# Optimization experiments

Measured on AMD Instinct MI355X. Metric: run time of the kernel, lower is better.

## Reference

```python
import jax, jax.numpy as jnp
import numpy as np

B, N1, N2, D, L, H = 2, 384, 384, 128, 3, 128
DM_MIN = 0.5


def _gat_layer(x, adj, W, Wb, A, gW, gb):
    # GAT_gate from jaechanglim/DTI_PDBbind: attention softmax over dim 1, gated residual
    h = x @ W + Wb                                   # [B,N,D]
    e = jnp.einsum('bjl,bkl->bjk', h @ A, h)
    e = e + jnp.swapaxes(e, 1, 2)
    att = jnp.where(adj > 0, e, -9e15)
    att = jax.nn.softmax(att, axis=1) * adj
    h_prime = jax.nn.relu(jnp.einsum('bij,bjk->bik', att, h))
    coeff = jax.nn.sigmoid(jnp.concatenate([x, h_prime], -1) @ gW + gb)  # [B,N,1]
    return coeff * x + (1.0 - coeff) * h_prime


def _pair_mlp(h1g, h2g, W1, b1, W2, b2):
    # MLP(concat(h1_i, h2_j)) without materializing the [B,N1,N2,2D] concat:
    # split W1 into ligand / protein halves and broadcast-add the projections.
    p1 = jnp.einsum('bnd,dk->bnk', h1g, W1[:D])      # [B,N1,H]
    p2 = jnp.einsum('bmd,dk->bmk', h2g, W1[D:])      # [B,N2,H]
    hid = jax.nn.relu(p1[:, :, None, :] + p2[:, None, :, :] + b1)  # [B,N1,N2,H]
    return (hid @ W2 + b2)[..., 0]                   # [B,N1,N2]


def reference(h1, adj1, h2, dmv, charge1, charge2, vdw_epsilon, vdw_sigma,
              delta_uff, valid1, valid2, no_metal1, no_metal2,
              node_W, gat_W, gat_Wb, gat_A, gat_gW, gat_gb,
              pair_W1, pair_b1, pair_W2, pair_b2,
              vdw_coeff, duff_coeff, int_W1, int_b1, int_W2, int_b2):
    h1g = h1 @ node_W
    h2g = h2 @ node_W
    for i in range(L):  # only ligand graph is convolved (as in the source)
        h1g = _gat_layer(h1g, adj1, gat_W[i], gat_Wb[i], gat_A[i], gat_gW[i], gat_gb[i])

    dm = jnp.sqrt(jnp.sum(dmv * dmv, -1) + 1e-10)    # [B,N1,N2]
    dm = jnp.where(dm < DM_MIN, 1e10, dm)

    # coulomb term (pair MLPs 0,1)
    cA = jax.nn.sigmoid(_pair_mlp(h1g, h2g, pair_W1[0], pair_b1[0], pair_W2[0], pair_b2[0]))
    cN = jax.nn.sigmoid(_pair_mlp(h1g, h2g, pair_W1[1], pair_b1[1], pair_W2[1], pair_b2[1])) * 2.0 + 1.0
    charge12 = charge1[:, :, None] * charge2[:, None, :]
    e_c = cA * charge12 * jnp.power(1.0 / dm, cN)
    e_c = e_c * valid1[:, :, None] * valid2[:, None, :]
    e_c = jnp.clip(e_c, -100.0, 100.0)
    e_c = jnp.sum(e_c, axis=(1, 2))[:, None]

    # vdw term (pair MLPs 2=A sigmoid, 3=B tanh, 4=N sigmoid)
    vA = (jax.nn.sigmoid(_pair_mlp(h1g, h2g, pair_W1[2], pair_b1[2], pair_W2[2], pair_b2[2])) * 0.6 + 0.7)
    vA = vA * (vdw_coeff[0] * vdw_coeff[0]) * vdw_epsilon
    vB = jnp.tanh(_pair_mlp(h1g, h2g, pair_W1[3], pair_b1[3], pair_W2[3], pair_b2[3])) * 0.6 + 0.7
    vN = jax.nn.sigmoid(_pair_mlp(h1g, h2g, pair_W1[4], pair_b1[4], pair_W2[4], pair_b2[4])) * 2.0 + 5.0
    dm0 = vdw_sigma * vB
    dm0 = jnp.where(dm0 < 1e-4, 1.0, dm0)
    r = jnp.power(dm0 / dm, vN)
    e_v = vA * (r * r - 2.0 * r)                     # (dm0/dm)^(2N) - 2(dm0/dm)^N
    e_v = e_v * no_metal1[:, :, None] * no_metal2[:, None, :]
    e_v = jnp.minimum(e_v, 100.0)
    e_v = jnp.sum(e_v, axis=(1, 2))[:, None]

    # conformational energy difference term
    e_u = (duff_coeff[0] * duff_coeff[0] * delta_uff)[:, None]

    # learned intercept from pooled ligand features
    hs = jnp.sum(h1g * valid1[..., None], axis=1)
    inter = jax.nn.relu(hs @ int_W1 + int_b1) @ int_W2 + int_b2

    return jnp.concatenate([e_c, e_v, e_u, inter], -1)  # [B,4]


def setup_inputs() -> dict:
    key = jax.random.key(0)
    ks = jax.random.split(key, 24)
    inp = {}
    inp['h1'] = jax.random.normal(ks[0], (B, N1, 54), jnp.float32)
    inp['h2'] = jax.random.normal(ks[1], (B, N2, 54), jnp.float32)
    a = jax.random.uniform(ks[2], (B, N1, N1))
    adj = (a > 0.9).astype(jnp.float32)
    adj = jnp.maximum(adj, jnp.swapaxes(adj, 1, 2))
    inp['adj1'] = jnp.maximum(adj, jnp.eye(N1, dtype=jnp.float32)[None])
    inp['dmv'] = jax.random.normal(ks[3], (B, N1, N2, 3), jnp.float32) * 3.0
    inp['charge1'] = jax.random.normal(ks[4], (B, N1), jnp.float32) * 0.3
    inp['charge2'] = jax.random.normal(ks[5], (B, N2), jnp.float32) * 0.3
    inp['vdw_epsilon'] = jax.random.uniform(ks[6], (B, N1, N2), jnp.float32) * 0.3
    inp['vdw_sigma'] = 3.0 + jax.random.uniform(ks[7], (B, N1, N2), jnp.float32)
    inp['delta_uff'] = jax.random.uniform(ks[8], (B,), jnp.float32) * 5.0
    inp['valid1'] = jnp.ones((B, N1), jnp.float32)
    inp['valid2'] = jnp.ones((B, N2), jnp.float32)
    inp['no_metal1'] = jnp.ones((B, N1), jnp.float32)
    inp['no_metal2'] = jnp.ones((B, N2), jnp.float32)
    # parameters
    inp['node_W'] = jax.random.normal(ks[9], (54, D), jnp.float32) * 0.1
    inp['gat_W'] = jax.random.normal(ks[10], (L, D, D), jnp.float32) * (1.0 / np.sqrt(D))
    inp['gat_Wb'] = jnp.zeros((L, D), jnp.float32)
    inp['gat_A'] = jax.random.normal(ks[11], (L, D, D), jnp.float32) * 0.05
    inp['gat_gW'] = jax.random.normal(ks[12], (L, 2 * D, 1), jnp.float32) * 0.05
    inp['gat_gb'] = jnp.zeros((L, 1), jnp.float32)
    inp['pair_W1'] = jax.random.normal(ks[13], (5, 2 * D, H), jnp.float32) * 0.05
    inp['pair_b1'] = jnp.zeros((5, H), jnp.float32)
    inp['pair_W2'] = jax.random.normal(ks[14], (5, H, 1), jnp.float32) * 0.1
    inp['pair_b2'] = jnp.zeros((5, 1), jnp.float32)
    inp['vdw_coeff'] = jnp.array([0.02], jnp.float32)
    inp['duff_coeff'] = jnp.array([0.1], jnp.float32)
    inp['int_W1'] = jax.random.normal(ks[15], (D, H), jnp.float32) * 0.05
    inp['int_b1'] = jnp.zeros((H,), jnp.float32)
    inp['int_W2'] = jax.random.normal(ks[16], (H, 1), jnp.float32) * 0.1
    inp['int_b2'] = jnp.zeros((1,), jnp.float32)
    return inp
```

## Files before the change

kernel.cpp:

```cpp
#include <hip/hip_runtime.h>
#include <math.h>

#define BB 2
#define NN 384
#define DD 128
#define HH 128
#define RT_ALL (BB * NN)
#define PCOLS (BB * NN)

__device__ __forceinline__ float sigmoidf_(float x) { return 1.f / (1.f + __expf(-x)); }
__device__ __forceinline__ float tanhf_(float x)    { return 1.f - 2.f / (__expf(2.f * x) + 1.f); }

__global__ __launch_bounds__(256) void k_embed(
    const float* __restrict__ h1, const float* __restrict__ h2,
    const float* __restrict__ nW, float* __restrict__ h1g, float* __restrict__ h2g) {
  int r0 = blockIdx.x * 2;
  int tid = threadIdx.x;
  const float* src; float* dst; int rb;
  if (r0 < RT_ALL) { src = h1; dst = h1g; rb = r0; }
  else             { src = h2; dst = h2g; rb = r0 - RT_ALL; }
  __shared__ float xs[2][54];
  if (tid < 108) xs[tid / 54][tid % 54] = src[rb * 54 + tid];
  __syncthreads();
  int rr = tid >> 7, c = tid & 127;
  float acc = 0.f;
#pragma unroll 6
  for (int k = 0; k < 54; ++k) acc += xs[rr][k] * nW[k * DD + c];
  dst[(rb + rr) * DD + c] = acc;
}

__global__ __launch_bounds__(256) void k_gat_hhA(
    const float* __restrict__ x, const float* __restrict__ W,
    const float* __restrict__ Wb, const float* __restrict__ A,
    float* __restrict__ h, float* __restrict__ hA,
    float* __restrict__ hT, float* __restrict__ hAT) {
  int r = blockIdx.x;
  int tid = threadIdx.x, c = tid & 127, kh = tid >> 7;
  __shared__ float xs[DD], hs[DD];
  __shared__ float ph[2][DD];
  if (tid < DD) xs[tid] = x[r * DD + tid];
  __syncthreads();
  float acc = 0.f;
  const float* Wp = W + (kh * 64) * DD + c;
#pragma unroll 4
  for (int k = 0; k < 64; ++k) acc += xs[kh * 64 + k] * Wp[k * DD];
  ph[kh][c] = acc;
  __syncthreads();
  if (tid < DD) {
    float hv = ph[0][tid] + ph[1][tid] + Wb[tid];
    h[r * DD + tid] = hv; hT[tid * PCOLS + r] = hv; hs[tid] = hv;
  }
  __syncthreads();
  acc = 0.f;
  const float* Ap = A + (kh * 64) * DD + c;
#pragma unroll 4
  for (int k = 0; k < 64; ++k) acc += hs[kh * 64 + k] * Ap[k * DD];
  ph[kh][c] = acc;
  __syncthreads();
  if (tid < DD) {
    float av = ph[0][tid] + ph[1][tid];
    hA[r * DD + tid] = av; hAT[tid * PCOLS + r] = av;
  }
}

__global__ __launch_bounds__(384) void k_gat_att(
    const float* __restrict__ h, const float* __restrict__ hA,
    const float* __restrict__ hT, const float* __restrict__ hAT,
    const float* __restrict__ adj, float* __restrict__ attT) {
  int col = blockIdx.x;
  int b = col / NN;
  int tid = threadIdx.x;
  const float* hrow  = h  + col * DD;
  const float* hArow = hA + col * DD;
  const float* hTb  = hT  + b * NN + tid;
  const float* hATb = hAT + b * NN + tid;
  float e = 0.f;
#pragma unroll 8
  for (int c = 0; c < DD; ++c)
    e += hATb[c * PCOLS] * hrow[c] + hTb[c * PCOLS] * hArow[c];
  float a = adj[col * NN + tid];
  __shared__ float rmx[6], rsm[6];
  float lmax = (a > 0.f) ? e : -3e38f;
#pragma unroll
  for (int off = 32; off > 0; off >>= 1) lmax = fmaxf(lmax, __shfl_down(lmax, off));
  if ((tid & 63) == 0) rmx[tid >> 6] = lmax;
  __syncthreads();
  float m = fmaxf(fmaxf(fmaxf(rmx[0], rmx[1]), fmaxf(rmx[2], rmx[3])), fmaxf(rmx[4], rmx[5]));
  float v = (a > 0.f) ? __expf(e - m) : 0.f;
  float s = v;
#pragma unroll
  for (int off = 32; off > 0; off >>= 1) s += __shfl_down(s, off);
  if ((tid & 63) == 0) rsm[tid >> 6] = s;
  __syncthreads();
  float inv = 1.f / (rsm[0] + rsm[1] + rsm[2] + rsm[3] + rsm[4] + rsm[5]);
  attT[col * NN + tid] = v * a * inv;
}

__global__ __launch_bounds__(256) void k_gat_out(
    const float* __restrict__ x, const float* __restrict__ h,
    const float* __restrict__ attT, const float* __restrict__ gW,
    const float* __restrict__ gb, float* __restrict__ out) {
  int r = blockIdx.x;
  int b = r / NN, i = r - b * NN;
  int tid = threadIdx.x, c = tid & 127, jh = tid >> 7;
  __shared__ float arow[NN];
  __shared__ float ph[2][DD];
  __shared__ float redw[2];
  for (int idx = tid; idx < NN; idx += 256) arow[idx] = attT[(b * NN + idx) * NN + i];
  __syncthreads();
  float acc = 0.f;
  const float* hp = h + (b * NN + jh * 192) * DD + c;
#pragma unroll 4
  for (int jj = 0; jj < 192; ++jj) acc += arow[jh * 192 + jj] * hp[jj * DD];
  ph[jh][c] = acc;
  __syncthreads();
  if (tid < DD) {
    float hpr = fmaxf(ph[0][tid] + ph[1][tid], 0.f);
    float xr = x[r * DD + tid];
    float v = xr * gW[tid] + hpr * gW[DD + tid];
#pragma unroll
    for (int off = 32; off > 0; off >>= 1) v += __shfl_down(v, off);
    if ((tid & 63) == 0) redw[tid >> 6] = v;
  }
  __syncthreads();
  if (tid < DD) {
    float hpr = fmaxf(ph[0][tid] + ph[1][tid], 0.f);
    float xr = x[r * DD + tid];
    float coeff = sigmoidf_(redw[0] + redw[1] + gb[0]);
    out[r * DD + tid] = coeff * xr + (1.f - coeff) * hpr;
  }
}

__global__ __launch_bounds__(256) void k_pair_proj(
    const float* __restrict__ h1g, const float* __restrict__ h2g,
    const float* __restrict__ W1, const float* __restrict__ b1,
    const float* __restrict__ delta_uff, const float* __restrict__ duff_coeff,
    float* __restrict__ p1, float* __restrict__ p2T, float* __restrict__ out) {
  const int RT = 16;
  int m = blockIdx.x % 5;
  int r0 = (blockIdx.x / 5) * RT;
  int tid = threadIdx.x, c = tid & 127, kh = tid >> 7;
  if (blockIdx.x == 0 && tid < BB * 4) {
    int bb = tid >> 2, cc = tid & 3;
    out[tid] = (cc == 2) ? duff_coeff[0] * duff_coeff[0] * delta_uff[bb] : 0.f;
  }
  bool lig = (r0 < RT_ALL);
  const float* src = lig ? h1g : h2g;
  int rb = lig ? r0 : r0 - RT_ALL;
  const float* W = W1 + (m * 256 + (lig ? 0 : 128)) * HH;
  __shared__ float xs[RT][DD];
  __shared__ float ps[RT][DD];
  for (int idx = tid; idx < RT * DD; idx += 256) xs[idx >> 7][idx & 127] = src[rb * DD + idx];
  __syncthreads();
  float acc[RT];
#pragma unroll
  for (int r = 0; r < RT; ++r) acc[r] = 0.f;
  const float* Wp = W + (kh * 64) * HH + c;
#pragma unroll 2
  for (int k = 0; k < 64; ++k) {
    float w = Wp[k * HH];
#pragma unroll
    for (int r = 0; r < RT; ++r) acc[r] += xs[r][kh * 64 + k] * w;
  }
  if (kh == 1) {
#pragma unroll
    for (int r = 0; r < RT; ++r) ps[r][c] = acc[r];
  }
  __syncthreads();
  if (kh == 0) {
    if (lig) {
      float bias = b1[m * HH + c];
#pragma unroll
      for (int r = 0; r < RT; ++r)
        p1[((rb + r) * 5 + m) * HH + c] = acc[r] + ps[r][c] + bias;
    } else {
      float* dst = p2T + (m * HH + c) * PCOLS + rb;
#pragma unroll
      for (int q = 0; q < RT / 4; ++q) {
        float4 v = make_float4(acc[4 * q + 0] + ps[4 * q + 0][c],
                               acc[4 * q + 1] + ps[4 * q + 1][c],
                               acc[4 * q + 2] + ps[4 * q + 2][c],
                               acc[4 * q + 3] + ps[4 * q + 3][c]);
        *(float4*)(dst + 4 * q) = v;
      }
    }
  }
}

__global__ __launch_bounds__(192) void k_pair_energy(
    const float* __restrict__ p1, const float* __restrict__ p2T,
    const float* __restrict__ W2, const float* __restrict__ b2,
    const float* __restrict__ dmv, const float* __restrict__ charge1,
    const float* __restrict__ charge2, const float* __restrict__ veps,
    const float* __restrict__ vsig, const float* __restrict__ valid1,
    const float* __restrict__ valid2, const float* __restrict__ nm1,
    const float* __restrict__ nm2, const float* __restrict__ vdw_coeff,
    const float* __restrict__ h1g, float* __restrict__ ws_int,
    float* __restrict__ out) {
  int tid = threadIdx.x;
  if (blockIdx.x >= 768) {
    int eb = blockIdx.x - 768;
    int b = eb >> 2, ch = eb & 3;
    if (tid < DD) {
      float acc = 0.f;
      int i0 = ch * 96;
#pragma unroll 4
      for (int i = 0; i < 96; ++i) {
        int gi = b * NN + i0 + i;
        acc += h1g[gi * DD + tid] * valid1[gi];
      }
      ws_int[eb * DD + tid] = acc;
    }
    return;
  }
  const int TI = 2;
  int tile = blockIdx.x >> 1, jh = blockIdx.x & 1;
  int r0 = tile * TI;
  int b = r0 / NN;
  int j = jh * 192 + tid;
  int col = b * NN + j;

  const float* q0 = p1 + (r0 + 0) * 5 * HH;
  const float* q1 = p1 + (r0 + 1) * 5 * HH;
  float acc0[5], acc1[5];
#pragma unroll
  for (int m = 0; m < 5; ++m) {
    const float* p2c = p2T + m * HH * PCOLS + col;
    const float* w2m = W2 + m * HH;
    const float* x0 = q0 + m * HH;
    const float* x1 = q1 + m * HH;
    float a0 = b2[m], a1 = b2[m];
#pragma unroll 8
    for (int h = 0; h < HH; ++h) {
      float pv = p2c[h * PCOLS];
      float w = w2m[h];
      a0 += fmaxf(x0[h] + pv, 0.f) * w;
      a1 += fmaxf(x1[h] + pv, 0.f) * w;
    }
    acc0[m] = a0; acc1[m] = a1;
  }

  float q2c = charge2[col], v2 = valid2[col], n2 = nm2[col];
  float vc2 = vdw_coeff[0] * vdw_coeff[0];
  float ec_sum = 0.f, ev_sum = 0.f;
#pragma unroll
  for (int ti = 0; ti < TI; ++ti) {
    const float* am = ti ? acc1 : acc0;
    int gi = r0 + ti;
    int pidx = gi * NN + j;
    float dx = dmv[pidx * 3 + 0], dy = dmv[pidx * 3 + 1], dz = dmv[pidx * 3 + 2];
    float dm = sqrtf(dx * dx + dy * dy + dz * dz + 1e-10f);
    if (dm < 0.5f) dm = 1e10f;
    float cA = sigmoidf_(am[0]);
    float cN = sigmoidf_(am[1]) * 2.f + 1.f;
    float e_c = cA * charge1[gi] * q2c * __powf(1.f / dm, cN);
    e_c *= valid1[gi] * v2;
    e_c = fminf(fmaxf(e_c, -100.f), 100.f);
    ec_sum += e_c;
    float vA = (sigmoidf_(am[2]) * 0.6f + 0.7f) * vc2 * veps[pidx];
    float vB = tanhf_(am[3]) * 0.6f + 0.7f;
    float vN = sigmoidf_(am[4]) * 2.f + 5.f;
    float dm0 = vsig[pidx] * vB;
    if (dm0 < 1e-4f) dm0 = 1.f;
    float rr = __powf(dm0 / dm, vN);
    float e_v = vA * (rr * rr - 2.f * rr);
    e_v *= nm1[gi] * n2;
    e_v = fminf(e_v, 100.f);
    ev_sum += e_v;
  }
#pragma unroll
  for (int off = 32; off > 0; off >>= 1) {
    ec_sum += __shfl_down(ec_sum, off);
    ev_sum += __shfl_down(ev_sum, off);
  }
  __shared__ float rec[3], rev[3];
  if ((tid & 63) == 0) { rec[tid >> 6] = ec_sum; rev[tid >> 6] = ev_sum; }
  __syncthreads();
  if (tid == 0) {
    atomicAdd(&out[b * 4 + 0], rec[0] + rec[1] + rec[2]);
    atomicAdd(&out[b * 4 + 1], rev[0] + rev[1] + rev[2]);
  }
}

__global__ __launch_bounds__(256) void k_intercept_fin(
    const float* __restrict__ ws_int, const float* __restrict__ W1,
    const float* __restrict__ b1, const float* __restrict__ W2,
    const float* __restrict__ b2, float* __restrict__ out) {
  int b = blockIdx.x;
  int tid = threadIdx.x, c = tid & 127, kh = tid >> 7;
  __shared__ float hsf[DD];
  __shared__ float ph[2][DD];
  __shared__ float redw[2];
  if (tid < DD)
    hsf[tid] = ws_int[(b * 4 + 0) * DD + tid] + ws_int[(b * 4 + 1) * DD + tid]
             + ws_int[(b * 4 + 2) * DD + tid] + ws_int[(b * 4 + 3) * DD + tid];
  __syncthreads();
  float acc = 0.f;
  const float* Wp = W1 + (kh * 64) * HH + c;
#pragma unroll 4
  for (int k = 0; k < 64; ++k) acc += hsf[kh * 64 + k] * Wp[k * HH];
  ph[kh][c] = acc;
  __syncthreads();
  if (tid < DD) {
    float hid = fmaxf(ph[0][tid] + ph[1][tid] + b1[tid], 0.f);
    float v = hid * W2[tid];
#pragma unroll
    for (int off = 32; off > 0; off >>= 1) v += __shfl_down(v, off);
    if ((tid & 63) == 0) redw[tid >> 6] = v;
  }
  __syncthreads();
  if (tid == 0) out[b * 4 + 3] = redw[0] + redw[1] + b2[0];
}

extern "C" void kernel_launch(void* const* d_in, const int* in_sizes, int n_in,
                              void* d_out, int out_size, void* d_ws, size_t ws_size,
                              hipStream_t stream) {
  (void)in_sizes; (void)n_in; (void)out_size; (void)ws_size;
  const float* h1         = (const float*)d_in[0];
  const float* h2         = (const float*)d_in[1];
  const float* adj1       = (const float*)d_in[2];
  const float* dmv        = (const float*)d_in[3];
  const float* charge1    = (const float*)d_in[4];
  const float* charge2    = (const float*)d_in[5];
  const float* veps       = (const float*)d_in[6];
  const float* vsig       = (const float*)d_in[7];
  const float* delta_uff  = (const float*)d_in[8];
  const float* valid1     = (const float*)d_in[9];
  const float* valid2     = (const float*)d_in[10];
  const float* nm1        = (const float*)d_in[11];
  const float* nm2        = (const float*)d_in[12];
  const float* node_W     = (const float*)d_in[13];
  const float* gat_W      = (const float*)d_in[14];
  const float* gat_Wb     = (const float*)d_in[15];
  const float* gat_A      = (const float*)d_in[16];
  const float* gat_gW     = (const float*)d_in[17];
  const float* gat_gb     = (const float*)d_in[18];
  const float* pW1        = (const float*)d_in[19];
  const float* pb1        = (const float*)d_in[20];
  const float* pW2        = (const float*)d_in[21];
  const float* pb2        = (const float*)d_in[22];
  const float* vdw_coeff  = (const float*)d_in[23];
  const float* duff_coeff = (const float*)d_in[24];
  const float* iW1        = (const float*)d_in[25];
  const float* ib1        = (const float*)d_in[26];
  const float* iW2        = (const float*)d_in[27];
  const float* ib2        = (const float*)d_in[28];
  float* out = (float*)d_out;

  float* ws = (float*)d_ws;
  const int RN = BB * NN * DD;
  float* h1gA   = ws;
  float* h1gB   = h1gA + RN;
  float* h2g    = h1gB + RN;
  float* hbuf   = h2g + RN;
  float* hAbuf  = hbuf + RN;
  float* hTbuf  = hAbuf + RN;
  float* hATbuf = hTbuf + RN;
  float* attT   = hATbuf + RN;
  float* p1     = attT + BB * NN * NN;
  float* p2T    = p1 + BB * NN * 5 * HH;
  float* ws_int = p2T + 5 * HH * PCOLS;

  k_embed<<<dim3(2 * BB * NN / 2), dim3(256), 0, stream>>>(h1, h2, node_W, h1gA, h2g);

  float* cur = h1gA;
  float* nxt = h1gB;
  for (int l = 0; l < 3; ++l) {
    k_gat_hhA<<<dim3(BB * NN), dim3(256), 0, stream>>>(
        cur, gat_W + l * DD * DD, gat_Wb + l * DD, gat_A + l * DD * DD,
        hbuf, hAbuf, hTbuf, hATbuf);
    k_gat_att<<<dim3(BB * NN), dim3(384), 0, stream>>>(
        hbuf, hAbuf, hTbuf, hATbuf, adj1, attT);
    k_gat_out<<<dim3(BB * NN), dim3(256), 0, stream>>>(
        cur, hbuf, attT, gat_gW + l * 2 * DD, gat_gb + l, nxt);
    float* t = cur; cur = nxt; nxt = t;
  }
  const float* h1gF = cur;

  k_pair_proj<<<dim3((2 * BB * NN / 16) * 5), dim3(256), 0, stream>>>(
      h1gF, h2g, pW1, pb1, delta_uff, duff_coeff, p1, p2T, out);
  k_pair_energy<<<dim3(768 + 8), dim3(192), 0, stream>>>(
      p1, p2T, pW2, pb2, dmv, charge1, charge2, veps, vsig,
      valid1, valid2, nm1, nm2, vdw_coeff, h1gF, ws_int, out);
  k_intercept_fin<<<dim3(BB), dim3(256), 0, stream>>>(ws_int, iW1, ib1, iW2, ib2, out);
}
```

Measured before the change: 325.7 us.

## Fuse all stages into one cooperative persistent kernel with grid syncs

Replaces the chain of about thirteen separate kernel launches with a single cooperative kernel of 256 blocks that moves from stage to stage using grid.sync(). Each stage is re-tiled so every block handles three or six rows, and the pair-energy stage reads the protein projection through a float4-interleaved layout. The aim is to remove launch gaps and per-launch overhead. In exchange the grid is small (256 blocks), each row's work is serialised across fewer threads, and every grid-wide barrier adds its own cost.

Result: slower. 761.1 us (+133.7%).

```diff
diff --git a/kernel.cpp b/kernel.cpp
--- a/kernel.cpp
+++ b/kernel.cpp
@@ -1,386 +1,385 @@
 #include <hip/hip_runtime.h>
+#include <hip/hip_cooperative_groups.h>
 #include <math.h>
 
-#define BB 2
+namespace cg = cooperative_groups;
+
 #define NN 384
 #define DD 128
 #define HH 128
-#define RT_ALL (BB * NN)
-#define PCOLS (BB * NN)
 
 __device__ __forceinline__ float sigmoidf_(float x) { return 1.f / (1.f + __expf(-x)); }
 __device__ __forceinline__ float tanhf_(float x)    { return 1.f - 2.f / (__expf(2.f * x) + 1.f); }
 
-__global__ __launch_bounds__(256) void k_embed(
-    const float* __restrict__ h1, const float* __restrict__ h2,
-    const float* __restrict__ nW, float* __restrict__ h1g, float* __restrict__ h2g) {
-  int r0 = blockIdx.x * 2;
-  int tid = threadIdx.x;
-  const float* src; float* dst; int rb;
-  if (r0 < RT_ALL) { src = h1; dst = h1g; rb = r0; }
-  else             { src = h2; dst = h2g; rb = r0 - RT_ALL; }
-  __shared__ float xs[2][54];
-  if (tid < 108) xs[tid / 54][tid % 54] = src[rb * 54 + tid];
-  __syncthreads();
-  int rr = tid >> 7, c = tid & 127;
-  float acc = 0.f;
+struct Params {
+  const float *h1, *h2, *adj1, *dmv, *charge1, *charge2, *veps, *vsig, *delta_uff;
+  const float *valid1, *valid2, *nm1, *nm2;
+  const float *node_W, *gat_W, *gat_Wb, *gat_A, *gat_gW, *gat_gb;
+  const float *pW1, *pb1, *pW2, *pb2, *vdw_coeff, *duff_coeff;
+  const float *iW1, *ib1, *iW2, *ib2;
+  float *out;
+  float *h1gA, *h1gB, *h2g, *hbuf, *hAbuf, *hTbuf, *hATbuf, *att, *p1, *p2q, *ws_int;
+};
+
+__global__ __launch_bounds__(384) void k_mega(Params P) {
+  cg::grid_group grid = cg::this_grid();
+  const int blk = blockIdx.x;
+  const int tid = threadIdx.x;
+  const int c = tid & 127;
+  const int g = tid >> 7;
+
+  if (blk == 0 && tid < 8) {
+    int bb = tid >> 2, cc = tid & 3;
+    P.out[tid] = (cc == 2) ? P.duff_coeff[0] * P.duff_coeff[0] * P.delta_uff[bb] : 0.f;
+  }
+  {
+    int rb = blk * 6;
+    for (int p = 0; p < 2; ++p) {
+      int r = rb + p * 3 + g;
+      const float* src; float* dst; int rr;
+      if (r < 768) { src = P.h1; dst = P.h1gA; rr = r; }
+      else         { src = P.h2; dst = P.h2g;  rr = r - 768; }
+      const float* xr = src + rr * 54;
+      float acc = 0.f;
 #pragma unroll 6
-  for (int k = 0; k < 54; ++k) acc += xs[rr][k] * nW[k * DD + c];
-  dst[(rb + rr) * DD + c] = acc;
-}
-
-__global__ __launch_bounds__(256) void k_gat_hhA(
-    const float* __restrict__ x, const float* __restrict__ W,
-    const float* __restrict__ Wb, const float* __restrict__ A,
-    float* __restrict__ h, float* __restrict__ hA,
-    float* __restrict__ hT, float* __restrict__ hAT) {
-  int r = blockIdx.x;
-  int tid = threadIdx.x, c = tid & 127, kh = tid >> 7;
-  __shared__ float xs[DD], hs[DD];
-  __shared__ float ph[2][DD];
-  if (tid < DD) xs[tid] = x[r * DD + tid];
-  __syncthreads();
-  float acc = 0.f;
-  const float* Wp = W + (kh * 64) * DD + c;
-#pragma unroll 4
-  for (int k = 0; k < 64; ++k) acc += xs[kh * 64 + k] * Wp[k * DD];
-  ph[kh][c] = acc;
-  __syncthreads();
-  if (tid < DD) {
-    float hv = ph[0][tid] + ph[1][tid] + Wb[tid];
-    h[r * DD + tid] = hv; hT[tid * PCOLS + r] = hv; hs[tid] = hv;
-  }
-  __syncthreads();
-  acc = 0.f;
-  const float* Ap = A + (kh * 64) * DD + c;
-#pragma unroll 4
-  for (int k = 0; k < 64; ++k) acc += hs[kh * 64 + k] * Ap[k * DD];
-  ph[kh][c] = acc;
-  __syncthreads();
-  if (tid < DD) {
-    float av = ph[0][tid] + ph[1][tid];
-    hA[r * DD + tid] = av; hAT[tid * PCOLS + r] = av;
-  }
-}
-
-__global__ __launch_bounds__(384) void k_gat_att(
-    const float* __restrict__ h, const float* __restrict__ hA,
-    const float* __restrict__ hT, const float* __restrict__ hAT,
-    const float* __restrict__ adj, float* __restrict__ attT) {
-  int col = blockIdx.x;
-  int b = col / NN;
-  int tid = threadIdx.x;
-  const float* hrow  = h  + col * DD;
-  const float* hArow = hA + col * DD;
-  const float* hTb  = hT  + b * NN + tid;
-  const float* hATb = hAT + b * NN + tid;
-  float e = 0.f;
-#pragma unroll 8
-  for (int c = 0; c < DD; ++c)
-    e += hATb[c * PCOLS] * hrow[c] + hTb[c * PCOLS] * hArow[c];
-  float a = adj[col * NN + tid];
-  __shared__ float rmx[6], rsm[6];
-  float lmax = (a > 0.f) ? e : -3e38f;
-#pragma unroll
-  for (int off = 32; off > 0; off >>= 1) lmax = fmaxf(lmax, __shfl_down(lmax, off));
-  if ((tid & 63) == 0) rmx[tid >> 6] = lmax;
-  __syncthreads();
-  float m = fmaxf(fmaxf(fmaxf(rmx[0], rmx[1]), fmaxf(rmx[2], rmx[3])), fmaxf(rmx[4], rmx[5]));
-  float v = (a > 0.f) ? __expf(e - m) : 0.f;
-  float s = v;
-#pragma unroll
-  for (int off = 32; off > 0; off >>= 1) s += __shfl_down(s, off);
-  if ((tid & 63) == 0) rsm[tid >> 6] = s;
-  __syncthreads();
-  float inv = 1.f / (rsm[0] + rsm[1] + rsm[2] + rsm[3] + rsm[4] + rsm[5]);
-  attT[col * NN + tid] = v * a * inv;
-}
-
-__global__ __launch_bounds__(256) void k_gat_out(
-    const float* __restrict__ x, const float* __restrict__ h,
-    const float* __restrict__ attT, const float* __restrict__ gW,
-    const float* __restrict__ gb, float* __restrict__ out) {
-  int r = blockIdx.x;
-  int b = r / NN, i = r - b * NN;
-  int tid = threadIdx.x, c = tid & 127, jh = tid >> 7;
-  __shared__ float arow[NN];
-  __shared__ float ph[2][DD];
-  __shared__ float redw[2];
-  for (int idx = tid; idx < NN; idx += 256) arow[idx] = attT[(b * NN + idx) * NN + i];
-  __syncthreads();
-  float acc = 0.f;
-  const float* hp = h + (b * NN + jh * 192) * DD + c;
-#pragma unroll 4
-  for (int jj = 0; jj < 192; ++jj) acc += arow[jh * 192 + jj] * hp[jj * DD];
-  ph[jh][c] = acc;
-  __syncthreads();
-  if (tid < DD) {
-    float hpr = fmaxf(ph[0][tid] + ph[1][tid], 0.f);
-    float xr = x[r * DD + tid];
-    float v = xr * gW[tid] + hpr * gW[DD + tid];
-#pragma unroll
-    for (int off = 32; off > 0; off >>= 1) v += __shfl_down(v, off);
-    if ((tid & 63) == 0) redw[tid >> 6] = v;
-  }
-  __syncthreads();
-  if (tid < DD) {
-    float hpr = fmaxf(ph[0][tid] + ph[1][tid], 0.f);
-    float xr = x[r * DD + tid];
-    float coeff = sigmoidf_(redw[0] + redw[1] + gb[0]);
-    out[r * DD + tid] = coeff * xr + (1.f - coeff) * hpr;
-  }
-}
-
-__global__ __launch_bounds__(256) void k_pair_proj(
-    const float* __restrict__ h1g, const float* __restrict__ h2g,
-    const float* __restrict__ W1, const float* __restrict__ b1,
-    const float* __restrict__ delta_uff, const float* __restrict__ duff_coeff,
-    float* __restrict__ p1, float* __restrict__ p2T, float* __restrict__ out) {
-  const int RT = 16;
-  int m = blockIdx.x % 5;
-  int r0 = (blockIdx.x / 5) * RT;
-  int tid = threadIdx.x, c = tid & 127, kh = tid >> 7;
-  if (blockIdx.x == 0 && tid < BB * 4) {
-    int bb = tid >> 2, cc = tid & 3;
-    out[tid] = (cc == 2) ? duff_coeff[0] * duff_coeff[0] * delta_uff[bb] : 0.f;
-  }
-  bool lig = (r0 < RT_ALL);
-  const float* src = lig ? h1g : h2g;
-  int rb = lig ? r0 : r0 - RT_ALL;
-  const float* W = W1 + (m * 256 + (lig ? 0 : 128)) * HH;
-  __shared__ float xs[RT][DD];
-  __shared__ float ps[RT][DD];
-  for (int idx = tid; idx < RT * DD; idx += 256) xs[idx >> 7][idx & 127] = src[rb * DD + idx];
-  __syncthreads();
-  float acc[RT];
-#pragma unroll
-  for (int r = 0; r < RT; ++r) acc[r] = 0.f;
-  const float* Wp = W + (kh * 64) * HH + c;
-#pragma unroll 2
-  for (int k = 0; k < 64; ++k) {
-    float w = Wp[k * HH];
-#pragma unroll
-    for (int r = 0; r < RT; ++r) acc[r] += xs[r][kh * 64 + k] * w;
-  }
-  if (kh == 1) {
-#pragma unroll
-    for (int r = 0; r < RT; ++r) ps[r][c] = acc[r];
-  }
-  __syncthreads();
-  if (kh == 0) {
-    if (lig) {
-      float bias = b1[m * HH + c];
-#pragma unroll
-      for (int r = 0; r < RT; ++r)
-        p1[((rb + r) * 5 + m) * HH + c] = acc[r] + ps[r][c] + bias;
-    } else {
-      float* dst = p2T + (m * HH + c) * PCOLS + rb;
-#pragma unroll
-      for (int q = 0; q < RT / 4; ++q) {
-        float4 v = make_float4(acc[4 * q + 0] + ps[4 * q + 0][c],
-                               acc[4 * q + 1] + ps[4 * q + 1][c],
-                               acc[4 * q + 2] + ps[4 * q + 2][c],
-                               acc[4 * q + 3] + ps[4 * q + 3][c]);
-        *(float4*)(dst + 4 * q) = v;
-      }
-    }
-  }
-}
-
-__global__ __launch_bounds__(192) void k_pair_energy(
-    const float* __restrict__ p1, const float* __restrict__ p2T,
-    const float* __restrict__ W2, const float* __restrict__ b2,
-    const float* __restrict__ dmv, const float* __restrict__ charge1,
-    const float* __restrict__ charge2, const float* __restrict__ veps,
-    const float* __restrict__ vsig, const float* __restrict__ valid1,
-    const float* __restrict__ valid2, const float* __restrict__ nm1,
-    const float* __restrict__ nm2, const float* __restrict__ vdw_coeff,
-    const float* __restrict__ h1g, float* __restrict__ ws_int,
-    float* __restrict__ out) {
-  int tid = threadIdx.x;
-  if (blockIdx.x >= 768) {
-    int eb = blockIdx.x - 768;
-    int b = eb >> 2, ch = eb & 3;
-    if (tid < DD) {
+      for (int k = 0; k < 54; ++k) acc += xr[k] * P.node_W[k * DD + c];
+      dst[rr * DD + c] = acc;
+    }
+  }
+  grid.sync();
+
+  float* cur = P.h1gA;
+  float* nxt = P.h1gB;
+  for (int l = 0; l < 3; ++l) {
+    const float* W  = P.gat_W  + l * DD * DD;
+    const float* Wb = P.gat_Wb + l * DD;
+    const float* A  = P.gat_A  + l * DD * DD;
+    const float* gW = P.gat_gW + l * 2 * DD;
+    const float* gb = P.gat_gb + l;
+
+    {
+      __shared__ float hs[3][DD];
+      int r = blk * 3 + g;
+      const float4* xr4 = (const float4*)(cur + r * DD);
+      float a0 = 0.f, a1 = 0.f;
+#pragma unroll 4
+      for (int k4 = 0; k4 < DD / 4; ++k4) {
+        float4 xv = xr4[k4];
+        int k = k4 * 4;
+        a0 += xv.x * W[k * DD + c] + xv.z * W[(k + 2) * DD + c];
+        a1 += xv.y * W[(k + 1) * DD + c] + xv.w * W[(k + 3) * DD + c];
+      }
+      float hv = a0 + a1 + Wb[c];
+      P.hbuf[r * DD + c] = hv;
+      P.hTbuf[c * 768 + r] = hv;
+      hs[g][c] = hv;
+      __syncthreads();
+      const float4* hs4 = (const float4*)hs[g];
+      a0 = 0.f; a1 = 0.f;
+#pragma unroll 4
+      for (int k4 = 0; k4 < DD / 4; ++k4) {
+        float4 xv = hs4[k4];
+        int k = k4 * 4;
+        a0 += xv.x * A[k * DD + c] + xv.z * A[(k + 2) * DD + c];
+        a1 += xv.y * A[(k + 1) * DD + c] + xv.w * A[(k + 3) * DD + c];
+      }
+      float av = a0 + a1;
+      P.hAbuf[r * DD + c] = av;
+      P.hATbuf[c * 768 + r] = av;
+    }
+    grid.sync();
+
+    {
+      __shared__ float red[3][6];
+      int b = blk >> 7;
+      int k0g = blk * 3;
+      int kk0 = k0g - b * NN;
+      int j = tid;
+      const float* hTb  = P.hTbuf  + b * NN + j;
+      const float* hATb = P.hATbuf + b * NN + j;
+      const float* h0r = P.hbuf  + (k0g + 0) * DD;
+      const float* h1r = P.hbuf  + (k0g + 1) * DD;
+      const float* h2r = P.hbuf  + (k0g + 2) * DD;
+      const float* a0r = P.hAbuf + (k0g + 0) * DD;
+      const float* a1r = P.hAbuf + (k0g + 1) * DD;
+      const float* a2r = P.hAbuf + (k0g + 2) * DD;
+      float e0 = 0.f, e1 = 0.f, e2 = 0.f;
+#pragma unroll 4
+      for (int cc = 0; cc < DD; ++cc) {
+        float tv = hTb[cc * 768], av = hATb[cc * 768];
+        e0 += av * h0r[cc] + tv * a0r[cc];
+        e1 += av * h1r[cc] + tv * a1r[cc];
+        e2 += av * h2r[cc] + tv * a2r[cc];
+      }
+      float aj0 = P.adj1[(k0g + 0) * NN + j];
+      float aj1 = P.adj1[(k0g + 1) * NN + j];
+      float aj2 = P.adj1[(k0g + 2) * NN + j];
+      float l0 = aj0 > 0.f ? e0 : -3e38f;
+      float l1 = aj1 > 0.f ? e1 : -3e38f;
+      float l2 = aj2 > 0.f ? e2 : -3e38f;
+#pragma unroll
+      for (int off = 32; off > 0; off >>= 1) {
+        l0 = fmaxf(l0, __shfl_down(l0, off));
+        l1 = fmaxf(l1, __shfl_down(l1, off));
+        l2 = fmaxf(l2, __shfl_down(l2, off));
+      }
+      int w = tid >> 6;
+      if ((tid & 63) == 0) { red[0][w] = l0; red[1][w] = l1; red[2][w] = l2; }
+      __syncthreads();
+      float m0 = red[0][0], m1 = red[1][0], m2 = red[2][0];
+#pragma unroll
+      for (int q = 1; q < 6; ++q) {
+        m0 = fmaxf(m0, red[0][q]); m1 = fmaxf(m1, red[1][q]); m2 = fmaxf(m2, red[2][q]);
+      }
+      float v0 = aj0 > 0.f ? __expf(e0 - m0) : 0.f;
+      float v1 = aj1 > 0.f ? __expf(e1 - m1) : 0.f;
+      float v2 = aj2 > 0.f ? __expf(e2 - m2) : 0.f;
+      float s0 = v0, s1 = v1, s2 = v2;
+#pragma unroll
+      for (int off = 32; off > 0; off >>= 1) {
+        s0 += __shfl_down(s0, off);
+        s1 += __shfl_down(s1, off);
+        s2 += __shfl_down(s2, off);
+      }
+      __syncthreads();
+      if ((tid & 63) == 0) { red[0][w] = s0; red[1][w] = s1; red[2][w] = s2; }
+      __syncthreads();
+      float d0 = 0.f, d1 = 0.f, d2 = 0.f;
+#pragma unroll
+      for (int q = 0; q < 6; ++q) { d0 += red[0][q]; d1 += red[1][q]; d2 += red[2][q]; }
+      float* arow = P.att + (b * NN + j) * NN + kk0;
+      arow[0] = v0 * aj0 / d0;
+      arow[1] = v1 * aj1 / d1;
+      arow[2] = v2 * aj2 / d2;
+    }
+    grid.sync();
+
+    {
+      __shared__ float redw[3][2];
+      int r = blk * 3 + g;
+      int b = blk >> 7;
+      const float4* ar4 = (const float4*)(P.att + r * NN);
+      const float* hp = P.hbuf + b * NN * DD + c;
+      float q0 = 0.f, q1 = 0.f, q2 = 0.f, q3 = 0.f;
+#pragma unroll 4
+      for (int j4 = 0; j4 < NN / 4; ++j4) {
+        float4 av = ar4[j4];
+        const float* hj = hp + j4 * 4 * DD;
+        q0 += av.x * hj[0];
+        q1 += av.y * hj[DD];
+        q2 += av.z * hj[2 * DD];
+        q3 += av.w * hj[3 * DD];
+      }
+      float hpr = fmaxf((q0 + q1) + (q2 + q3), 0.f);
+      float xr = cur[r * DD + c];
+      float v = xr * gW[c] + hpr * gW[DD + c];
+#pragma unroll
+      for (int off = 32; off > 0; off >>= 1) v += __shfl_down(v, off);
+      if ((tid & 63) == 0) redw[g][(tid >> 6) & 1] = v;
+      __syncthreads();
+      float coeff = sigmoidf_(redw[g][0] + redw[g][1] + gb[0]);
+      nxt[r * DD + c] = coeff * xr + (1.f - coeff) * hpr;
+    }
+    { float* t = cur; cur = nxt; nxt = t; }
+    grid.sync();
+  }
+
+  {
+    bool lig = blk < 128;
+    int rbase = lig ? blk * 6 : blk * 6 - 768;
+    const float* src = lig ? cur : P.h2g;
+    const float* xbase = src + rbase * DD;
+    for (int pass = 0; pass < 2; ++pass) {
+      int o = tid + pass * 384;
+      if (o < 640) {
+        int m = o >> 7, hc = o & 127;
+        const float* Wcol = P.pW1 + (m * 256 + (lig ? 0 : 128)) * HH + hc;
+        float acc[6] = {0.f, 0.f, 0.f, 0.f, 0.f, 0.f};
+#pragma unroll 4
+        for (int k = 0; k < DD; ++k) {
+          float w = Wcol[k * HH];
+#pragma unroll
+          for (int r = 0; r < 6; ++r) acc[r] += xbase[r * DD + k] * w;
+        }
+        if (lig) {
+          float bias = P.pb1[m * HH + hc];
+#pragma unroll
+          for (int r = 0; r < 6; ++r)
+            P.p1[((rbase + r) * 5 + m) * HH + hc] = acc[r] + bias;
+        } else {
+          float* dst = P.p2q + (size_t)((m * 32 + (hc >> 2)) * 768 + rbase) * 4 + (hc & 3);
+#pragma unroll
+          for (int r = 0; r < 6; ++r) dst[4 * r] = acc[r];
+        }
+      }
+    }
+  }
+  grid.sync();
+
+  {
+    int b = blk >> 7;
+    int r0 = blk * 3;
+    int j = tid;
+    int col = b * NN + j;
+    const float* q0 = P.p1 + (r0 + 0) * 640;
+    const float* q1 = P.p1 + (r0 + 1) * 640;
+    const float* q2 = P.p1 + (r0 + 2) * 640;
+    const float4* p2q4 = (const float4*)P.p2q;
+    float am[3][5];
+#pragma unroll
+    for (int m = 0; m < 5; ++m) {
+      const float4* pc = p2q4 + (size_t)(m * 32) * 768 + col;
+      const float* w2m = P.pW2 + m * HH;
+      const float* x0 = q0 + m * HH;
+      const float* x1 = q1 + m * HH;
+      const float* x2 = q2 + m * HH;
+      float a0 = 0.f, a1 = 0.f, a2 = 0.f;
+#pragma unroll 4
+      for (int hq = 0; hq < 32; ++hq) {
+        float4 pv = pc[(size_t)hq * 768];
+        float w0 = w2m[4 * hq], w1 = w2m[4 * hq + 1], w2v = w2m[4 * hq + 2], w3 = w2m[4 * hq + 3];
+        a0 += fmaxf(x0[4 * hq] + pv.x, 0.f) * w0 + fmaxf(x0[4 * hq + 1] + pv.y, 0.f) * w1
+            + fmaxf(x0[4 * hq + 2] + pv.z, 0.f) * w2v + fmaxf(x0[4 * hq + 3] + pv.w, 0.f) * w3;
+        a1 += fmaxf(x1[4 * hq] + pv.x, 0.f) * w0 + fmaxf(x1[4 * hq + 1] + pv.y, 0.f) * w1
+            + fmaxf(x1[4 * hq + 2] + pv.z, 0.f) * w2v + fmaxf(x1[4 * hq + 3] + pv.w, 0.f) * w3;
+        a2 += fmaxf(x2[4 * hq] + pv.x, 0.f) * w0 + fmaxf(x2[4 * hq + 1] + pv.y, 0.f) * w1
+            + fmaxf(x2[4 * hq + 2] + pv.z, 0.f) * w2v + fmaxf(x2[4 * hq + 3] + pv.w, 0.f) * w3;
+      }
+      float bb = P.pb2[m];
+      am[0][m] = a0 + bb; am[1][m] = a1 + bb; am[2][m] = a2 + bb;
+    }
+
+    float q2c = P.charge2[col], vv2 = P.valid2[col], n2 = P.nm2[col];
+    float vc2 = P.vdw_coeff[0] * P.vdw_coeff[0];
+    float ec_sum = 0.f, ev_sum = 0.f;
+#pragma unroll
+    for (int ti = 0; ti < 3; ++ti) {
+      int gi = r0 + ti;
+      int pidx = gi * NN + j;
+      float dx = P.dmv[pidx * 3], dy = P.dmv[pidx * 3 + 1], dz = P.dmv[pidx * 3 + 2];
+      float dm = sqrtf(dx * dx + dy * dy + dz * dz + 1e-10f);
+      if (dm < 0.5f) dm = 1e10f;
+      float cA = sigmoidf_(am[ti][0]);
+      float cN = sigmoidf_(am[ti][1]) * 2.f + 1.f;
+      float e_c = cA * P.charge1[gi] * q2c * __powf(1.f / dm, cN);
+      e_c *= P.valid1[gi] * vv2;
+      e_c = fminf(fmaxf(e_c, -100.f), 100.f);
+      ec_sum += e_c;
+      float vA = (sigmoidf_(am[ti][2]) * 0.6f + 0.7f) * vc2 * P.veps[pidx];
+      float vB = tanhf_(am[ti][3]) * 0.6f + 0.7f;
+      float vN = sigmoidf_(am[ti][4]) * 2.f + 5.f;
+      float dm0 = P.vsig[pidx] * vB;
+      if (dm0 < 1e-4f) dm0 = 1.f;
+      float rr = __powf(dm0 / dm, vN);
+      float e_v = vA * (rr * rr - 2.f * rr);
+      e_v *= P.nm1[gi] * n2;
+      e_v = fminf(e_v, 100.f);
+      ev_sum += e_v;
+    }
+#pragma unroll
+    for (int off = 32; off > 0; off >>= 1) {
+      ec_sum += __shfl_down(ec_sum, off);
+      ev_sum += __shfl_down(ev_sum, off);
+    }
+    __shared__ float rec[6], rev[6];
+    if ((tid & 63) == 0) { rec[tid >> 6] = ec_sum; rev[tid >> 6] = ev_sum; }
+    __syncthreads();
+    if (tid == 0) {
+      float a = 0.f, cc = 0.f;
+#pragma unroll
+      for (int w = 0; w < 6; ++w) { a += rec[w]; cc += rev[w]; }
+      atomicAdd(&P.out[b * 4 + 0], a);
+      atomicAdd(&P.out[b * 4 + 1], cc);
+    }
+    if (blk < 8 && tid < DD) {
+      int bb = blk >> 2, ch = blk & 3;
       float acc = 0.f;
       int i0 = ch * 96;
 #pragma unroll 4
       for (int i = 0; i < 96; ++i) {
-        int gi = b * NN + i0 + i;
-        acc += h1g[gi * DD + tid] * valid1[gi];
-      }
-      ws_int[eb * DD + tid] = acc;
-    }
-    return;
-  }
-  const int TI = 2;
-  int tile = blockIdx.x >> 1, jh = blockIdx.x & 1;
-  int r0 = tile * TI;
-  int b = r0 / NN;
-  int j = jh * 192 + tid;
-  int col = b * NN + j;
-
-  const float* q0 = p1 + (r0 + 0) * 5 * HH;
-  const float* q1 = p1 + (r0 + 1) * 5 * HH;
-  float acc0[5], acc1[5];
-#pragma unroll
-  for (int m = 0; m < 5; ++m) {
-    const float* p2c = p2T + m * HH * PCOLS + col;
-    const float* w2m = W2 + m * HH;
-    const float* x0 = q0 + m * HH;
-    const float* x1 = q1 + m * HH;
-    float a0 = b2[m], a1 = b2[m];
-#pragma unroll 8
-    for (int h = 0; h < HH; ++h) {
-      float pv = p2c[h * PCOLS];
-      float w = w2m[h];
-      a0 += fmaxf(x0[h] + pv, 0.f) * w;
-      a1 += fmaxf(x1[h] + pv, 0.f) * w;
-    }
-    acc0[m] = a0; acc1[m] = a1;
-  }
-
-  float q2c = charge2[col], v2 = valid2[col], n2 = nm2[col];
-  float vc2 = vdw_coeff[0] * vdw_coeff[0];
-  float ec_sum = 0.f, ev_sum = 0.f;
-#pragma unroll
-  for (int ti = 0; ti < TI; ++ti) {
-    const float* am = ti ? acc1 : acc0;
-    int gi = r0 + ti;
-    int pidx = gi * NN + j;
-    float dx = dmv[pidx * 3 + 0], dy = dmv[pidx * 3 + 1], dz = dmv[pidx * 3 + 2];
-    float dm = sqrtf(dx * dx + dy * dy + dz * dz + 1e-10f);
-    if (dm < 0.5f) dm = 1e10f;
-    float cA = sigmoidf_(am[0]);
-    float cN = sigmoidf_(am[1]) * 2.f + 1.f;
-    float e_c = cA * charge1[gi] * q2c * __powf(1.f / dm, cN);
-    e_c *= valid1[gi] * v2;
-    e_c = fminf(fmaxf(e_c, -100.f), 100.f);
-    ec_sum += e_c;
-    float vA = (sigmoidf_(am[2]) * 0.6f + 0.7f) * vc2 * veps[pidx];
-    float vB = tanhf_(am[3]) * 0.6f + 0.7f;
-    float vN = sigmoidf_(am[4]) * 2.f + 5.f;
-    float dm0 = vsig[pidx] * vB;
-    if (dm0 < 1e-4f) dm0 = 1.f;
-    float rr = __powf(dm0 / dm, vN);
-    float e_v = vA * (rr * rr - 2.f * rr);
-    e_v *= nm1[gi] * n2;
-    e_v = fminf(e_v, 100.f);
-    ev_sum += e_v;
-  }
-#pragma unroll
-  for (int off = 32; off > 0; off >>= 1) {
-    ec_sum += __shfl_down(ec_sum, off);
-    ev_sum += __shfl_down(ev_sum, off);
-  }
-  __shared__ float rec[3], rev[3];
-  if ((tid & 63) == 0) { rec[tid >> 6] = ec_sum; rev[tid >> 6] = ev_sum; }
-  __syncthreads();
-  if (tid == 0) {
-    atomicAdd(&out[b * 4 + 0], rec[0] + rec[1] + rec[2]);
-    atomicAdd(&out[b * 4 + 1], rev[0] + rev[1] + rev[2]);
-  }
-}
-
-__global__ __launch_bounds__(256) void k_intercept_fin(
-    const float* __restrict__ ws_int, const float* __restrict__ W1,
-    const float* __restrict__ b1, const float* __restrict__ W2,
-    const float* __restrict__ b2, float* __restrict__ out) {
-  int b = blockIdx.x;
-  int tid = threadIdx.x, c = tid & 127, kh = tid >> 7;
-  __shared__ float hsf[DD];
-  __shared__ float ph[2][DD];
-  __shared__ float redw[2];
-  if (tid < DD)
-    hsf[tid] = ws_int[(b * 4 + 0) * DD + tid] + ws_int[(b * 4 + 1) * DD + tid]
-             + ws_int[(b * 4 + 2) * DD + tid] + ws_int[(b * 4 + 3) * DD + tid];
-  __syncthreads();
-  float acc = 0.f;
-  const float* Wp = W1 + (kh * 64) * HH + c;
-#pragma unroll 4
-  for (int k = 0; k < 64; ++k) acc += hsf[kh * 64 + k] * Wp[k * HH];
-  ph[kh][c] = acc;
-  __syncthreads();
-  if (tid < DD) {
-    float hid = fmaxf(ph[0][tid] + ph[1][tid] + b1[tid], 0.f);
-    float v = hid * W2[tid];
-#pragma unroll
-    for (int off = 32; off > 0; off >>= 1) v += __shfl_down(v, off);
-    if ((tid & 63) == 0) redw[tid >> 6] = v;
-  }
-  __syncthreads();
-  if (tid == 0) out[b * 4 + 3] = redw[0] + redw[1] + b2[0];
+        int gi = bb * NN + i0 + i;
+        acc += cur[gi * DD + tid] * P.valid1[gi];
+      }
+      P.ws_int[blk * DD + tid] = acc;
+    }
+  }
+  grid.sync();
+
+  if (blk == 0) {
+    __shared__ float hsf[2][DD];
+    __shared__ float redf[2][2];
+    int bb = tid >> 7;
+    int cc2 = tid & 127;
+    if (bb < 2) {
+      hsf[bb][cc2] = P.ws_int[(bb * 4 + 0) * DD + cc2] + P.ws_int[(bb * 4 + 1) * DD + cc2]
+                   + P.ws_int[(bb * 4 + 2) * DD + cc2] + P.ws_int[(bb * 4 + 3) * DD + cc2];
+    }
+    __syncthreads();
+    if (bb < 2) {
+      float hid = P.ib1[cc2];
+#pragma unroll 4
+      for (int k = 0; k < DD; ++k) hid += hsf[bb][k] * P.iW1[k * HH + cc2];
+      hid = fmaxf(hid, 0.f);
+      float v = hid * P.iW2[cc2];
+#pragma unroll
+      for (int off = 32; off > 0; off >>= 1) v += __shfl_down(v, off);
+      if ((tid & 63) == 0) redf[bb][(tid >> 6) & 1] = v;
+    }
+    __syncthreads();
+    if (tid < 2) P.out[tid * 4 + 3] = redf[tid][0] + redf[tid][1] + P.ib2[0];
+  }
 }
 
 extern "C" void kernel_launch(void* const* d_in, const int* in_sizes, int n_in,
                               void* d_out, int out_size, void* d_ws, size_t ws_size,
                               hipStream_t stream) {
   (void)in_sizes; (void)n_in; (void)out_size; (void)ws_size;
-  const float* h1         = (const float*)d_in[0];
-  const float* h2         = (const float*)d_in[1];
-  const float* adj1       = (const float*)d_in[2];
-  const float* dmv        = (const float*)d_in[3];
-  const float* charge1    = (const float*)d_in[4];
-  const float* charge2    = (const float*)d_in[5];
-  const float* veps       = (const float*)d_in[6];
-  const float* vsig       = (const float*)d_in[7];
-  const float* delta_uff  = (const float*)d_in[8];
-  const float* valid1     = (const float*)d_in[9];
-  const float* valid2     = (const float*)d_in[10];
-  const float* nm1        = (const float*)d_in[11];
-  const float* nm2        = (const float*)d_in[12];
-  const float* node_W     = (const float*)d_in[13];
-  const float* gat_W      = (const float*)d_in[14];
-  const float* gat_Wb     = (const float*)d_in[15];
-  const float* gat_A      = (const float*)d_in[16];
-  const float* gat_gW     = (const float*)d_in[17];
-  const float* gat_gb     = (const float*)d_in[18];
-  const float* pW1        = (const float*)d_in[19];
-  const float* pb1        = (const float*)d_in[20];
-  const float* pW2        = (const float*)d_in[21];
-  const float* pb2        = (const float*)d_in[22];
-  const float* vdw_coeff  = (const float*)d_in[23];
-  const float* duff_coeff = (const float*)d_in[24];
-  const float* iW1        = (const float*)d_in[25];
-  const float* ib1        = (const float*)d_in[26];
-  const float* iW2        = (const float*)d_in[27];
-  const float* ib2        = (const float*)d_in[28];
-  float* out = (float*)d_out;
+  Params P;
+  P.h1         = (const float*)d_in[0];
+  P.h2         = (const float*)d_in[1];
+  P.adj1       = (const float*)d_in[2];
+  P.dmv        = (const float*)d_in[3];
+  P.charge1    = (const float*)d_in[4];
+  P.charge2    = (const float*)d_in[5];
+  P.veps       = (const float*)d_in[6];
+  P.vsig       = (const float*)d_in[7];
+  P.delta_uff  = (const float*)d_in[8];
+  P.valid1     = (const float*)d_in[9];
+  P.valid2     = (const float*)d_in[10];
+  P.nm1        = (const float*)d_in[11];
+  P.nm2        = (const float*)d_in[12];
+  P.node_W     = (const float*)d_in[13];
+  P.gat_W      = (const float*)d_in[14];
+  P.gat_Wb     = (const float*)d_in[15];
+  P.gat_A      = (const float*)d_in[16];
+  P.gat_gW     = (const float*)d_in[17];
+  P.gat_gb     = (const float*)d_in[18];
+  P.pW1        = (const float*)d_in[19];
+  P.pb1        = (const float*)d_in[20];
+  P.pW2        = (const float*)d_in[21];
+  P.pb2        = (const float*)d_in[22];
+  P.vdw_coeff  = (const float*)d_in[23];
+  P.duff_coeff = (const float*)d_in[24];
+  P.iW1        = (const float*)d_in[25];
+  P.ib1        = (const float*)d_in[26];
+  P.iW2        = (const float*)d_in[27];
+  P.ib2        = (const float*)d_in[28];
+  P.out = (float*)d_out;
 
   float* ws = (float*)d_ws;
-  const int RN = BB * NN * DD;
-  float* h1gA   = ws;
-  float* h1gB   = h1gA + RN;
-  float* h2g    = h1gB + RN;
-  float* hbuf   = h2g + RN;
-  float* hAbuf  = hbuf + RN;
-  float* hTbuf  = hAbuf + RN;
-  float* hATbuf = hTbuf + RN;
-  float* attT   = hATbuf + RN;
-  float* p1     = attT + BB * NN * NN;
-  float* p2T    = p1 + BB * NN * 5 * HH;
-  float* ws_int = p2T + 5 * HH * PCOLS;
-
-  k_embed<<<dim3(2 * BB * NN / 2), dim3(256), 0, stream>>>(h1, h2, node_W, h1gA, h2g);
-
-  float* cur = h1gA;
-  float* nxt = h1gB;
-  for (int l = 0; l < 3; ++l) {
-    k_gat_hhA<<<dim3(BB * NN), dim3(256), 0, stream>>>(
-        cur, gat_W + l * DD * DD, gat_Wb + l * DD, gat_A + l * DD * DD,
-        hbuf, hAbuf, hTbuf, hATbuf);
-    k_gat_att<<<dim3(BB * NN), dim3(384), 0, stream>>>(
-        hbuf, hAbuf, hTbuf, hATbuf, adj1, attT);
-    k_gat_out<<<dim3(BB * NN), dim3(256), 0, stream>>>(
-        cur, hbuf, attT, gat_gW + l * 2 * DD, gat_gb + l, nxt);
-    float* t = cur; cur = nxt; nxt = t;
-  }
-  const float* h1gF = cur;
-
-  k_pair_proj<<<dim3((2 * BB * NN / 16) * 5), dim3(256), 0, stream>>>(
-      h1gF, h2g, pW1, pb1, delta_uff, duff_coeff, p1, p2T, out);
-  k_pair_energy<<<dim3(768 + 8), dim3(192), 0, stream>>>(
-      p1, p2T, pW2, pb2, dmv, charge1, charge2, veps, vsig,
-      valid1, valid2, nm1, nm2, vdw_coeff, h1gF, ws_int, out);
-  k_intercept_fin<<<dim3(BB), dim3(256), 0, stream>>>(ws_int, iW1, ib1, iW2, ib2, out);
+  const int RN = 768 * DD;
+  P.h1gA   = ws;
+  P.h1gB   = P.h1gA + RN;
+  P.h2g    = P.h1gB + RN;
+  P.hbuf   = P.h2g + RN;
+  P.hAbuf  = P.hbuf + RN;
+  P.hTbuf  = P.hAbuf + RN;
+  P.hATbuf = P.hTbuf + RN;
+  P.att    = P.hATbuf + RN;
+  P.p1     = P.att + 2 * NN * NN;
+  P.p2q    = P.p1 + 768 * 640;
+  P.ws_int = P.p2q + 768 * 640;
+
+  void* args[] = { &P };
+  hipLaunchCooperativeKernel((const void*)k_mega, dim3(256), dim3(384), args, 0, stream);
 }
```
